# Kernel optimization log

Hardware: AMD Instinct MI355X
Metric: run time of the kernel (lower is better)

The kernel has to match this reference:

```python
import jax, jax.numpy as jnp
import numpy as np

B, N, C, H = 8, 2048, 512, 8
D = C // H  # head_dim = 64

def rope(t):
    # t: (B, H, T, D); rotate even/odd interleaved pairs
    T = t.shape[2]
    inv_freq = 1.0 / (10000.0 ** (jnp.arange(0, D, 2, dtype=t.dtype) / D))  # (D/2,)
    pos = jnp.arange(T, dtype=t.dtype)
    freqs = pos[:, None] * inv_freq[None, :]            # (T, D/2)
    cos, sin = jnp.cos(freqs), jnp.sin(freqs)           # broadcast over (B,H)
    t_un = t[..., 0::2]
    t_ev = t[..., 1::2]
    r_un = t_un * cos - t_ev * sin
    r_ev = t_un * sin + t_ev * cos
    # interleave back: (..., D/2, 2) -> (..., D)
    return jnp.stack([r_un, r_ev], axis=-1).reshape(t.shape)

def setup_inputs() -> dict:
    key = jax.random.key(0)
    k1, k2, k3, k4 = jax.random.split(key, 4)
    x = jax.random.normal(k1, (B, N, C), dtype=jnp.float32)
    mask = jax.random.normal(k2, (B, N), dtype=jnp.float32)
    W_qkv = jax.random.normal(k3, (3 * C, C), dtype=jnp.float32) * (1.0 / np.sqrt(C))
    W_proj = jax.random.normal(k4, (C, C), dtype=jnp.float32) * (1.0 / np.sqrt(C))
    b_proj = jnp.zeros((C,), dtype=jnp.float32)
    return {"x": x, "mask": mask, "W_qkv": W_qkv, "W_proj": W_proj,
            "b_proj": b_proj, "num_cls_token": 1}

def reference(x, mask, W_qkv, W_proj, b_proj, num_cls_token):
    scale = D ** (-0.5)
    qkv = jnp.einsum('bnc,fc->bnf', x, W_qkv)             # (B,N,3C)
    qkv = qkv.reshape(B, N, 3, H, D).transpose(2, 0, 3, 1, 4)  # (3,B,H,N,D)
    q, k, v = qkv[0], qkv[1], qkv[2]
    nc = num_cls_token
    if nc > 0:
        q = jnp.concatenate([q[:, :, :nc], rope(q[:, :, nc:])], axis=2)
        k = jnp.concatenate([k[:, :, :nc], rope(k[:, :, nc:])], axis=2)
    else:
        q, k = rope(q), rope(k)
    attn = jnp.einsum('bhnd,bhmd->bhnm', q * scale, k)    # (B,H,N,N)
    attn = attn + mask[:, None, None, :] + mask[:, None, :, None]
    attn = jax.nn.softmax(attn, axis=-1)
    out = jnp.einsum('bhnm,bhmd->bhnd', attn, v)          # (B,H,N,D)
    out = out.transpose(0, 2, 1, 3).reshape(B, N, C)
    return out @ W_proj.T + b_proj
```

## Files before the change

kernel.cpp:

```cpp
#include <hip/hip_runtime.h>
#include <cmath>

#define BB 8
#define NN 2048
#define CC 512
#define HH 8
#define DD 64
#define FF 1536
#define MM (BB*NN)

typedef _Float16 half_t;
typedef __attribute__((ext_vector_type(8))) _Float16 half8;
typedef __attribute__((ext_vector_type(4))) _Float16 half4;
typedef __attribute__((ext_vector_type(4))) float floatx4;
typedef __attribute__((ext_vector_type(16))) float floatx16;
typedef __attribute__((ext_vector_type(4))) float fx4;

#define LOG2E 1.44269504088896f

typedef const __attribute__((address_space(1))) unsigned int* gas_ptr;
typedef __attribute__((address_space(3))) unsigned int* las_ptr;
__device__ __forceinline__ void gld16(const half_t* g, half_t* l) {
  __builtin_amdgcn_global_load_lds((gas_ptr)g, (las_ptr)l, 16, 0, 0);
}

__global__ __launch_bounds__(256) void cvt_kernel(
    const float* __restrict__ s, half_t* __restrict__ d, int n8) {
  int i = blockIdx.x * 256 + threadIdx.x;
  if (i < n8) {
    float4 a = ((const float4*)s)[i * 2], b = ((const float4*)s)[i * 2 + 1];
    half8 h;
    h[0] = (half_t)a.x; h[1] = (half_t)a.y; h[2] = (half_t)a.z; h[3] = (half_t)a.w;
    h[4] = (half_t)b.x; h[5] = (half_t)b.y; h[6] = (half_t)b.z; h[7] = (half_t)b.w;
    ((half8*)d)[i] = h;
  }
}

__global__ __launch_bounds__(256) void qkv_mfma_kernel(
    const half_t* __restrict__ Ah,
    const half_t* __restrict__ Bh,
    const int*   __restrict__ ncp,
    half_t* __restrict__ Qh, half_t* __restrict__ Kh, half_t* __restrict__ Vt)
{
  __shared__ union {
    struct { half_t A[128 * 32]; half_t B[128 * 32]; } s;
    half_t T[4][64 * 68];
  } sm;

  const int tid  = threadIdx.x;
  const int wave = tid >> 6, lane = tid & 63;
  const int L15  = lane & 15, quad = lane >> 4;
  const int wm = (wave & 1) * 64, wn = (wave >> 1) * 64;
  const int m0 = blockIdx.x * 128;
  const int f0 = blockIdx.y * 128;

  const int srow = lane >> 2;
  const int scolh = (lane & 3) * 8;
  const half_t* Ag = Ah + (size_t)(m0 + wave * 16 + srow) * CC + scolh;
  const half_t* Bg = Bh + (size_t)(f0 + wave * 16 + srow) * CC + scolh;
  half_t* Al = &sm.s.A[(wave * 16) * 32];
  half_t* Bl = &sm.s.B[(wave * 16) * 32];

  floatx4 acc[4][4];
#pragma unroll
  for (int i = 0; i < 4; ++i)
#pragma unroll
    for (int j = 0; j < 4; ++j) acc[i][j] = (floatx4){0.f, 0.f, 0.f, 0.f};

  for (int k0 = 0; k0 < CC; k0 += 32) {
    __syncthreads();
    gld16(Ag + k0,            Al);
    gld16(Ag + k0 + 64 * CC,  Al + 64 * 32);
    gld16(Bg + k0,            Bl);
    gld16(Bg + k0 + 64 * CC,  Bl + 64 * 32);
    __syncthreads();
    half8 af[4], bf[4];
#pragma unroll
    for (int mi = 0; mi < 4; ++mi)
      af[mi] = *(const half8*)&sm.s.A[(wm + mi * 16 + L15) * 32 + quad * 8];
#pragma unroll
    for (int ni = 0; ni < 4; ++ni)
      bf[ni] = *(const half8*)&sm.s.B[(wn + ni * 16 + L15) * 32 + quad * 8];
#pragma unroll
    for (int mi = 0; mi < 4; ++mi)
#pragma unroll
      for (int ni = 0; ni < 4; ++ni)
        acc[mi][ni] = __builtin_amdgcn_mfma_f32_16x16x32_f16(af[mi], bf[ni], acc[mi][ni], 0, 0, 0);
  }

  const int which = f0 >> 9;
  const int b     = m0 >> 11;
  const int n_base = (m0 & 2047) + wm;

  if (which < 2) {
    const int nc = *ncp;
    half_t* dst = which ? Kh : Qh;
    const float qscale = which ? 1.0f : (0.125f * LOG2E);
#pragma unroll
    for (int ni = 0; ni < 4; ++ni) {
      const int f = f0 + wn + ni * 16 + L15;
      const int h = (f >> 6) & 7;
      const int d = f & 63;
      const float invf = __powf(10000.0f, -(float)(d & ~1) * (1.0f / 64.0f));
      const float sgn = (d & 1) ? 1.0f : -1.0f;
#pragma unroll
      for (int mi = 0; mi < 4; ++mi)
#pragma unroll
        for (int r = 0; r < 4; ++r) {
          const int n = n_base + mi * 16 + quad * 4 + r;
          float v = acc[mi][ni][r];
          float p = __shfl_xor(v, 1, 64);
          if (n >= nc) {
            float sv, cv;
            __sincosf((float)(n - nc) * invf, &sv, &cv);
            v = v * cv + sgn * p * sv;
          }
          dst[(((size_t)(b * HH + h) * NN + n) << 6) + d] = (half_t)(v * qscale);
        }
    }
  } else {
    __syncthreads();
#pragma unroll
    for (int ni = 0; ni < 4; ++ni)
#pragma unroll
      for (int mi = 0; mi < 4; ++mi)
#pragma unroll
        for (int r = 0; r < 4; ++r)
          sm.T[wave][(ni * 16 + L15) * 68 + mi * 16 + quad * 4 + r] = (half_t)acc[mi][ni][r];
    __syncthreads();
    const int h = ((f0 + wn) >> 6) & 7;
    const size_t gbase = ((size_t)(b * HH + h) * DD + lane) * NN + n_base;
#pragma unroll
    for (int c = 0; c < 8; ++c)
      *(half8*)(Vt + gbase + c * 8) = *(const half8*)&sm.T[wave][lane * 68 + c * 8];
  }
}

#define EXP2_OFF 4.3280851f
__global__ __launch_bounds__(256, 4) void flash_mfma_kernel(
    const half_t* __restrict__ Qh,
    const half_t* __restrict__ Kh,
    const half_t* __restrict__ Vt,
    const float*  __restrict__ mask,
    half_t* __restrict__ O)
{
  __shared__ half_t KV[2][2][64 * 64];

  const int tid  = threadIdx.x;
  const int wave = tid >> 6;
  const int lane = tid & 63;
  const int l31  = lane & 31;
  const int hi   = lane >> 5;
  const int l7   = lane & 7;

  const int bid  = blockIdx.x;
  const int xcd  = bid & 7;
  const int slot = bid >> 3;
  const int qt   = slot & 15;
  const int head = (slot >> 4) * 8 + xcd;
  const int b    = head >> 3;
  const int h    = head & 7;

  const half_t* Kt_base = Kh + ((((size_t)b * HH + h) * NN) << 6);
  const half_t* Vt_base = Vt + (((size_t)b * HH + h) * DD) * NN;

  half8 qf[4];
  {
    const half_t* Qp =
        Qh + ((((size_t)b * HH + h) * NN + qt * 128 + wave * 32 + l31) << 6) + hi * 8;
#pragma unroll
    for (int kd = 0; kd < 4; ++kd) qf[kd] = *(const half8*)(Qp + kd * 16);
  }

  const int r8  = lane >> 3;
  const int dof = ((l7 ^ r8) << 3);
  const half_t* kbase = Kt_base + (((size_t)(wave * 16 + r8)) << 6) + dof;
  const half_t* vbase = Vt_base + (size_t)(wave * 16 + r8) * NN + dof;

  int adK[4], adV[4];
#pragma unroll
  for (int c = 0; c < 4; ++c) {
    adK[c] = l31 * 128 + ((((c << 1) | hi) ^ l7) << 4);
    adV[c] = 8192 + l31 * 128 + ((((c << 1) | hi) ^ l7) << 4);
  }
  const char* L = (const char*)KV;

  floatx16 acc[2];
#pragma unroll
  for (int dt = 0; dt < 2; ++dt)
#pragma unroll
    for (int r = 0; r < 16; ++r) acc[dt][r] = 0.f;
  float l_part = 0.f;

  const float* mkb = mask + (size_t)b * NN + hi * 4;

#define STAGE(c, koff, voff)                                                  \
  {                                                                           \
    gld16(kbase + (koff),          &KV[c][0][wave * 1024]);                   \
    gld16(kbase + (koff) + 512,    &KV[c][0][wave * 1024 + 512]);             \
    gld16(vbase + (voff),          &KV[c][1][wave * 1024]);                   \
    gld16(vbase + (voff) + 8 * NN, &KV[c][1][wave * 1024 + 512]);             \
  }

#define COMPUTE(c, moff)                                                      \
  _Pragma("unroll")                                                           \
  for (int t = 0; t < 2; ++t) {                                               \
    fx4 m4[4];                                                                \
    _Pragma("unroll")                                                         \
    for (int r2 = 0; r2 < 4; ++r2)                                            \
      m4[r2] = *(const fx4*)(mkb + (moff) + t * 32 + r2 * 8);                 \
    floatx16 S;                                                               \
    _Pragma("unroll") for (int r = 0; r < 16; ++r) S[r] = 0.f;                \
    __builtin_amdgcn_s_setprio(1);                                            \
    _Pragma("unroll")                                                         \
    for (int kd = 0; kd < 4; ++kd) {                                          \
      half8 kf = *(const half8*)(L + (adK[kd] + (c) * 16384 + t * 4096));     \
      S = __builtin_amdgcn_mfma_f32_32x32x16_f16(kf, qf[kd], S, 0, 0, 0);     \
    }                                                                         \
    __builtin_amdgcn_s_setprio(0);                                            \
    _Pragma("unroll")                                                         \
    for (int r = 0; r < 16; ++r) {                                            \
      float p = __builtin_amdgcn_exp2f(fmaf(m4[r >> 2][r & 3], LOG2E, S[r] - EXP2_OFF)); \
      l_part += p;                                                            \
      S[r] = p;                                                               \
    }                                                                         \
    unsigned W[4][2];                                                         \
    _Pragma("unroll")                                                         \
    for (int r2 = 0; r2 < 4; ++r2)                                            \
      _Pragma("unroll")                                                       \
      for (int u = 0; u < 2; ++u) {                                           \
        union { half_t hh[2]; unsigned w; } pk;                               \
        pk.hh[0] = (half_t)S[r2 * 4 + 2 * u];                                 \
        pk.hh[1] = (half_t)S[r2 * 4 + 2 * u + 1];                             \
        W[r2][u] = pk.w;                                                      \
      }                                                                       \
    _Pragma("unroll")                                                         \
    for (int ksl = 0; ksl < 2; ++ksl) {                                       \
      unsigned A0 = W[2 * ksl][0],     A1 = W[2 * ksl][1];                    \
      unsigned B0 = W[2 * ksl + 1][0], B1 = W[2 * ksl + 1][1];                \
      unsigned pA0 = __shfl_xor(A0, 32, 64), pA1 = __shfl_xor(A1, 32, 64);    \
      unsigned pB0 = __shfl_xor(B0, 32, 64), pB1 = __shfl_xor(B1, 32, 64);    \
      union { unsigned u4[4]; half8 v; } pw;                                  \
      pw.u4[0] = hi ? pB0 : A0;                                               \
      pw.u4[1] = hi ? pB1 : A1;                                               \
      pw.u4[2] = hi ? B0 : pA0;                                               \
      pw.u4[3] = hi ? B1 : pA1;                                               \
      const int ks = t * 2 + ksl;                                             \
      __builtin_amdgcn_s_setprio(1);                                          \
      _Pragma("unroll")                                                       \
      for (int dt = 0; dt < 2; ++dt) {                                        \
        half8 vf = *(const half8*)(L + (adV[ks] + (c) * 16384 + dt * 4096));  \
        acc[dt] = __builtin_amdgcn_mfma_f32_32x32x16_f16(pw.v, vf, acc[dt], 0, 0, 0); \
      }                                                                       \
      __builtin_amdgcn_s_setprio(0);                                          \
    }                                                                         \
  }

  STAGE(0, 0, 0)
  STAGE(1, 4096, 64)
  asm volatile("s_waitcnt vmcnt(4)");
  __builtin_amdgcn_s_barrier();
  __builtin_amdgcn_sched_barrier(0);
  kbase += 8192; vbase += 128;

#pragma unroll 1
  for (int kt2 = 0; kt2 < 15; ++kt2) {
    COMPUTE(0, 0)
    __builtin_amdgcn_sched_barrier(0);
    __builtin_amdgcn_s_barrier();
    STAGE(0, 0, 0)
    asm volatile("s_waitcnt vmcnt(4)");
    __builtin_amdgcn_s_barrier();
    __builtin_amdgcn_sched_barrier(0);

    COMPUTE(1, 64)
    __builtin_amdgcn_sched_barrier(0);
    __builtin_amdgcn_s_barrier();
    STAGE(1, 4096, 64)
    asm volatile("s_waitcnt vmcnt(4)");
    __builtin_amdgcn_s_barrier();
    __builtin_amdgcn_sched_barrier(0);

    kbase += 8192; vbase += 128;
    mkb += 128;
  }

  COMPUTE(0, 0)
  asm volatile("s_waitcnt vmcnt(0)");
  __builtin_amdgcn_s_barrier();
  __builtin_amdgcn_sched_barrier(0);
  COMPUTE(1, 64)

#undef STAGE
#undef COMPUTE

  l_part += __shfl_xor(l_part, 32, 64);

  const size_t orow = (size_t)b * NN + qt * 128 + wave * 32;
#pragma unroll
  for (int r = 0; r < 16; ++r) {
    const int ql  = (r & 3) + 8 * (r >> 2) + 4 * hi;
    const float iv = 1.0f / __shfl(l_part, ql, 64);
    const size_t ro = ((orow + ql) << 9) + (h << 6) + l31;
    O[ro]      = (half_t)(acc[0][r] * iv);
    O[ro + 32] = (half_t)(acc[1][r] * iv);
  }
}

__global__ __launch_bounds__(256) void proj_mfma_kernel(
    const half_t* __restrict__ Ah,
    const half_t* __restrict__ Bh,
    const float* __restrict__ bias,
    float* __restrict__ out)
{
  __shared__ half_t As[128 * 32];
  __shared__ half_t Bs[128 * 32];

  const int tid  = threadIdx.x;
  const int wave = tid >> 6, lane = tid & 63;
  const int L15  = lane & 15, quad = lane >> 4;
  const int wm = (wave & 1) * 64, wn = (wave >> 1) * 64;
  const int m0 = blockIdx.x * 128;
  const int f0 = blockIdx.y * 128;

  const int srow = lane >> 2;
  const int scolh = (lane & 3) * 8;
  const half_t* Ag = Ah + (size_t)(m0 + wave * 16 + srow) * CC + scolh;
  const half_t* Bg = Bh + (size_t)(f0 + wave * 16 + srow) * CC + scolh;
  half_t* Al = &As[(wave * 16) * 32];
  half_t* Bl = &Bs[(wave * 16) * 32];

  floatx4 acc[4][4];
#pragma unroll
  for (int i = 0; i < 4; ++i)
#pragma unroll
    for (int j = 0; j < 4; ++j) acc[i][j] = (floatx4){0.f, 0.f, 0.f, 0.f};

  for (int k0 = 0; k0 < CC; k0 += 32) {
    __syncthreads();
    gld16(Ag + k0,           Al);
    gld16(Ag + k0 + 64 * CC, Al + 64 * 32);
    gld16(Bg + k0,           Bl);
    gld16(Bg + k0 + 64 * CC, Bl + 64 * 32);
    __syncthreads();
    half8 af[4], bf[4];
#pragma unroll
    for (int mi = 0; mi < 4; ++mi)
      af[mi] = *(const half8*)&As[(wm + mi * 16 + L15) * 32 + quad * 8];
#pragma unroll
    for (int ni = 0; ni < 4; ++ni)
      bf[ni] = *(const half8*)&Bs[(wn + ni * 16 + L15) * 32 + quad * 8];
#pragma unroll
    for (int mi = 0; mi < 4; ++mi)
#pragma unroll
      for (int ni = 0; ni < 4; ++ni)
        acc[mi][ni] = __builtin_amdgcn_mfma_f32_16x16x32_f16(af[mi], bf[ni], acc[mi][ni], 0, 0, 0);
  }

#pragma unroll
  for (int ni = 0; ni < 4; ++ni) {
    const int f = f0 + wn + ni * 16 + L15;
    const float bv = bias[f];
#pragma unroll
    for (int mi = 0; mi < 4; ++mi)
#pragma unroll
      for (int r = 0; r < 4; ++r)
        out[(size_t)(m0 + wm + mi * 16 + quad * 4 + r) * CC + f] = acc[mi][ni][r] + bv;
  }
}

extern "C" void kernel_launch(void* const* d_in, const int* in_sizes, int n_in,
                              void* d_out, int out_size, void* d_ws, size_t ws_size,
                              hipStream_t stream) {
  const float* x     = (const float*)d_in[0];
  const float* mask  = (const float*)d_in[1];
  const float* Wqkv  = (const float*)d_in[2];
  const float* Wproj = (const float*)d_in[3];
  const float* bproj = (const float*)d_in[4];
  const int*   ncp   = (const int*)d_in[5];
  float* out = (float*)d_out;

  const size_t per = (size_t)BB * HH * NN * DD;
  half_t* xh  = (half_t*)d_ws;
  half_t* Wqh = xh + (size_t)MM * CC;
  half_t* Wph = Wqh + (size_t)FF * CC;
  half_t* Qh  = Wph + (size_t)CC * CC;
  half_t* Kh  = Qh + per;
  half_t* Vt  = Kh + per;
  half_t* Oh  = Vt + per;

  cvt_kernel<<<dim3(MM * CC / 8 / 256), 256, 0, stream>>>(x, xh, MM * CC / 8);
  cvt_kernel<<<dim3(FF * CC / 8 / 256), 256, 0, stream>>>(Wqkv, Wqh, FF * CC / 8);
  cvt_kernel<<<dim3(CC * CC / 8 / 256), 256, 0, stream>>>(Wproj, Wph, CC * CC / 8);

  qkv_mfma_kernel<<<dim3(MM / 128, FF / 128), 256, 0, stream>>>(xh, Wqh, ncp, Qh, Kh, Vt);
  flash_mfma_kernel<<<dim3(BB * HH * (NN / 128)), 256, 0, stream>>>(Qh, Kh, Vt, mask, Oh);
  proj_mfma_kernel<<<dim3(MM / 128, CC / 128), 256, 0, stream>>>(Oh, Wph, bproj, out);
}
```

Measured before the change: 270.8 us.

## Merge conversion launches, precompute RoPE table, shrink projection tile width

```diff
diff --git a/kernel.cpp b/kernel.cpp
--- a/kernel.cpp
+++ b/kernel.cpp
@@ -17,6 +17,7 @@
 typedef __attribute__((ext_vector_type(4))) float fx4;
 
 #define LOG2E 1.44269504088896f
+#define EXP2_OFF 4.3280851f
 
 typedef const __attribute__((address_space(1))) unsigned int* gas_ptr;
 typedef __attribute__((address_space(3))) unsigned int* las_ptr;
@@ -24,22 +25,38 @@
   __builtin_amdgcn_global_load_lds((gas_ptr)g, (las_ptr)l, 16, 0, 0);
 }
 
-__global__ __launch_bounds__(256) void cvt_kernel(
-    const float* __restrict__ s, half_t* __restrict__ d, int n8) {
+#define N1 (MM * CC / 8)
+#define N2 (FF * CC / 8)
+#define N3 (CC * CC / 8)
+__global__ __launch_bounds__(256) void cvt_all_kernel(
+    const float* __restrict__ x, const float* __restrict__ wq,
+    const float* __restrict__ wp, half_t* __restrict__ d) {
   int i = blockIdx.x * 256 + threadIdx.x;
-  if (i < n8) {
-    float4 a = ((const float4*)s)[i * 2], b = ((const float4*)s)[i * 2 + 1];
-    half8 h;
-    h[0] = (half_t)a.x; h[1] = (half_t)a.y; h[2] = (half_t)a.z; h[3] = (half_t)a.w;
-    h[4] = (half_t)b.x; h[5] = (half_t)b.y; h[6] = (half_t)b.z; h[7] = (half_t)b.w;
-    ((half8*)d)[i] = h;
-  }
+  const float* s;
+  if (i < N1)            s = x  + (size_t)i * 8;
+  else if (i < N1 + N2)  s = wq + (size_t)(i - N1) * 8;
+  else                   s = wp + (size_t)(i - N1 - N2) * 8;
+  float4 a = ((const float4*)s)[0], b = ((const float4*)s)[1];
+  half8 h;
+  h[0] = (half_t)a.x; h[1] = (half_t)a.y; h[2] = (half_t)a.z; h[3] = (half_t)a.w;
+  h[4] = (half_t)b.x; h[5] = (half_t)b.y; h[6] = (half_t)b.z; h[7] = (half_t)b.w;
+  ((half8*)d)[i] = h;
+}
+
+__global__ __launch_bounds__(256) void rope_tab_kernel(float2* __restrict__ tab) {
+  int i = blockIdx.x * 256 + threadIdx.x;
+  int p = i >> 5, j = i & 31;
+  float ang = (float)p * __powf(10000.0f, -(float)(2 * j) * (1.0f / 64.0f));
+  float sv, cv;
+  __sincosf(ang, &sv, &cv);
+  tab[i] = make_float2(cv, sv);
 }
 
 __global__ __launch_bounds__(256) void qkv_mfma_kernel(
     const half_t* __restrict__ Ah,
     const half_t* __restrict__ Bh,
     const int*   __restrict__ ncp,
+    const float2* __restrict__ tab,
     half_t* __restrict__ Qh, half_t* __restrict__ Kh, half_t* __restrict__ Vt)
 {
   __shared__ union {
@@ -101,8 +118,8 @@
       const int f = f0 + wn + ni * 16 + L15;
       const int h = (f >> 6) & 7;
       const int d = f & 63;
-      const float invf = __powf(10000.0f, -(float)(d & ~1) * (1.0f / 64.0f));
       const float sgn = (d & 1) ? 1.0f : -1.0f;
+      const float2* tj = tab + (d >> 1);
 #pragma unroll
       for (int mi = 0; mi < 4; ++mi)
 #pragma unroll
@@ -111,9 +128,8 @@
           float v = acc[mi][ni][r];
           float p = __shfl_xor(v, 1, 64);
           if (n >= nc) {
-            float sv, cv;
-            __sincosf((float)(n - nc) * invf, &sv, &cv);
-            v = v * cv + sgn * p * sv;
+            float2 cs = tj[(size_t)(n - nc) * 32];
+            v = v * cs.x + sgn * p * cs.y;
           }
           dst[(((size_t)(b * HH + h) * NN + n) << 6) + d] = (half_t)(v * qscale);
         }
@@ -136,7 +152,6 @@
   }
 }
 
-#define EXP2_OFF 4.3280851f
 __global__ __launch_bounds__(256, 4) void flash_mfma_kernel(
     const half_t* __restrict__ Qh,
     const half_t* __restrict__ Kh,
@@ -314,14 +329,14 @@
     float* __restrict__ out)
 {
   __shared__ half_t As[128 * 32];
-  __shared__ half_t Bs[128 * 32];
+  __shared__ half_t Bs[64 * 32];
 
   const int tid  = threadIdx.x;
   const int wave = tid >> 6, lane = tid & 63;
   const int L15  = lane & 15, quad = lane >> 4;
-  const int wm = (wave & 1) * 64, wn = (wave >> 1) * 64;
+  const int wm = (wave & 1) * 64, wn = (wave >> 1) * 32;
   const int m0 = blockIdx.x * 128;
-  const int f0 = blockIdx.y * 128;
+  const int f0 = blockIdx.y * 64;
 
   const int srow = lane >> 2;
   const int scolh = (lane & 3) * 8;
@@ -330,35 +345,34 @@
   half_t* Al = &As[(wave * 16) * 32];
   half_t* Bl = &Bs[(wave * 16) * 32];
 
-  floatx4 acc[4][4];
+  floatx4 acc[4][2];
 #pragma unroll
   for (int i = 0; i < 4; ++i)
 #pragma unroll
-    for (int j = 0; j < 4; ++j) acc[i][j] = (floatx4){0.f, 0.f, 0.f, 0.f};
+    for (int j = 0; j < 2; ++j) acc[i][j] = (floatx4){0.f, 0.f, 0.f, 0.f};
 
   for (int k0 = 0; k0 < CC; k0 += 32) {
     __syncthreads();
     gld16(Ag + k0,           Al);
     gld16(Ag + k0 + 64 * CC, Al + 64 * 32);
     gld16(Bg + k0,           Bl);
-    gld16(Bg + k0 + 64 * CC, Bl + 64 * 32);
-    __syncthreads();
-    half8 af[4], bf[4];
+    __syncthreads();
+    half8 af[4], bf[2];
 #pragma unroll
     for (int mi = 0; mi < 4; ++mi)
       af[mi] = *(const half8*)&As[(wm + mi * 16 + L15) * 32 + quad * 8];
 #pragma unroll
-    for (int ni = 0; ni < 4; ++ni)
+    for (int ni = 0; ni < 2; ++ni)
       bf[ni] = *(const half8*)&Bs[(wn + ni * 16 + L15) * 32 + quad * 8];
 #pragma unroll
     for (int mi = 0; mi < 4; ++mi)
 #pragma unroll
-      for (int ni = 0; ni < 4; ++ni)
+      for (int ni = 0; ni < 2; ++ni)
         acc[mi][ni] = __builtin_amdgcn_mfma_f32_16x16x32_f16(af[mi], bf[ni], acc[mi][ni], 0, 0, 0);
   }
 
 #pragma unroll
-  for (int ni = 0; ni < 4; ++ni) {
+  for (int ni = 0; ni < 2; ++ni) {
     const int f = f0 + wn + ni * 16 + L15;
     const float bv = bias[f];
 #pragma unroll
@@ -388,12 +402,12 @@
   half_t* Kh  = Qh + per;
   half_t* Vt  = Kh + per;
   half_t* Oh  = Vt + per;
-
-  cvt_kernel<<<dim3(MM * CC / 8 / 256), 256, 0, stream>>>(x, xh, MM * CC / 8);
-  cvt_kernel<<<dim3(FF * CC / 8 / 256), 256, 0, stream>>>(Wqkv, Wqh, FF * CC / 8);
-  cvt_kernel<<<dim3(CC * CC / 8 / 256), 256, 0, stream>>>(Wproj, Wph, CC * CC / 8);
-
-  qkv_mfma_kernel<<<dim3(MM / 128, FF / 128), 256, 0, stream>>>(xh, Wqh, ncp, Qh, Kh, Vt);
+  float2* tab = (float2*)(Oh + per);
+
+  rope_tab_kernel<<<dim3(NN * 32 / 256), 256, 0, stream>>>(tab);
+  cvt_all_kernel<<<dim3((N1 + N2 + N3) / 256), 256, 0, stream>>>(x, Wqkv, Wproj, xh);
+
+  qkv_mfma_kernel<<<dim3(MM / 128, FF / 128), 256, 0, stream>>>(xh, Wqh, ncp, tab, Qh, Kh, Vt);
   flash_mfma_kernel<<<dim3(BB * HH * (NN / 128)), 256, 0, stream>>>(Qh, Kh, Vt, mask, Oh);
-  proj_mfma_kernel<<<dim3(MM / 128, CC / 128), 256, 0, stream>>>(Oh, Wph, bproj, out);
-}
+  proj_mfma_kernel<<<dim3(MM / 128, CC / 64), 256, 0, stream>>>(Oh, Wph, bproj, out);
+}
```

Result: slower. 337.3 us (+24.5%).
